# Kernel tuning notes

Hardware: AMD Instinct MI355X
Metric: run time of the kernel (lower is better)

Reference implementation:

```python
import jax, jax.numpy as jnp
import numpy as np
from jax import lax

# Model hyperparameters (match init_kwargs + Mamba2 defaults: ngroups=1, d_conv=4)
B_, IN_DIM, L_ = 4, 128, 2048
D_MODEL, OUT_DIM, D_STATE, K_SAME = 256, 128, 16, 4
EXPAND, HEADDIM, D_CONV = 3, 3, 4
D_INNER = EXPAND * D_MODEL            # 768
NHEADS = D_INNER // HEADDIM           # 256
CONV_DIM = D_INNER + 2 * D_STATE      # 800 (x, B, C go through depthwise conv)
D_IN_PROJ = 2 * D_INNER + 2 * D_STATE + NHEADS  # 1824 (z, xBC, dt)
EPS = 1e-5
DN = ('NCH', 'OIH', 'NCH')


def setup_inputs() -> dict:
    key = jax.random.key(0)
    ks = jax.random.split(key, 12)
    s = lambda f: 1.0 / np.sqrt(f)
    x = jax.random.normal(ks[0], (B_, IN_DIM, L_), jnp.float32)
    conv_w = jax.random.normal(ks[1], (D_MODEL, IN_DIM, K_SAME), jnp.float32) * s(IN_DIM * K_SAME)
    conv_b = jax.random.normal(ks[2], (D_MODEL,), jnp.float32) * 0.02
    in_proj_w = jax.random.normal(ks[3], (D_MODEL, D_IN_PROJ), jnp.float32) * s(D_MODEL)
    dw_conv_w = jax.random.normal(ks[4], (CONV_DIM, D_CONV), jnp.float32) * s(D_CONV)
    dw_conv_b = jax.random.normal(ks[5], (CONV_DIM,), jnp.float32) * 0.02
    dt_bias = jax.random.normal(ks[6], (NHEADS,), jnp.float32) * 0.5
    A_log = jnp.log(jax.random.uniform(ks[7], (NHEADS,), jnp.float32, 1.0, 16.0))
    D = 1.0 + jax.random.normal(ks[8], (NHEADS,), jnp.float32) * 0.1
    norm_w = jnp.ones((D_INNER,), jnp.float32)
    mamba_out_w = jax.random.normal(ks[9], (D_INNER, D_MODEL), jnp.float32) * s(D_INNER)
    out_conv_w = jax.random.normal(ks[10], (OUT_DIM, D_MODEL, K_SAME), jnp.float32) * s(D_MODEL * K_SAME)
    return dict(x=x, conv_w=conv_w, conv_b=conv_b, in_proj_w=in_proj_w,
                dw_conv_w=dw_conv_w, dw_conv_b=dw_conv_b, dt_bias=dt_bias,
                A_log=A_log, D=D, norm_w=norm_w, mamba_out_w=mamba_out_w,
                out_conv_w=out_conv_w)


def _ssd_scan(dt, A, Bm, Cm, xs):
    """Selective state-space recurrence.
    dt: [B,L,H]  A: [H]  Bm,Cm: [B,L,N]  xs: [B,L,H,P]  ->  y: [B,L,H,P]"""
    dA = jnp.exp(dt * A)  # [B,L,H]

    def step(h, inp):  # h: [B,H,P,N]
        dA_t, dt_t, B_t, C_t, x_t = inp
        dBx = (dt_t[:, :, None] * x_t)[..., None] * B_t[:, None, None, :]  # [B,H,P,N]
        h = h * dA_t[:, :, None, None] + dBx
        y = jnp.einsum('bhpn,bn->bhp', h, C_t)
        return h, y

    inputs = (dA.transpose(1, 0, 2), dt.transpose(1, 0, 2),
              Bm.transpose(1, 0, 2), Cm.transpose(1, 0, 2), xs.transpose(1, 0, 2, 3))
    h0 = jnp.zeros((dt.shape[0], NHEADS, HEADDIM, D_STATE), dt.dtype)
    _, ys = lax.scan(step, h0, inputs)
    return ys.transpose(1, 0, 2, 3)


def reference(x, conv_w, conv_b, in_proj_w, dw_conv_w, dw_conv_b, dt_bias,
              A_log, D, norm_w, mamba_out_w, out_conv_w):
    B, _, L = x.shape
    # Conv1d padding='same' with even kernel k=4: torch pads (left=1, right=2)
    h = lax.conv_general_dilated(x, conv_w, (1,), [(1, 2)], dimension_numbers=DN)
    h = h + conv_b[None, :, None]
    u = h.transpose(0, 2, 1)  # [B,L,d_model]

    zxbcdt = u @ in_proj_w  # [B,L,1824]
    z = zxbcdt[..., :D_INNER]
    xBC = zxbcdt[..., D_INNER:D_INNER + CONV_DIM]
    dt = zxbcdt[..., D_INNER + CONV_DIM:]  # [B,L,H]
    dt = jax.nn.softplus(dt + dt_bias)

    # causal depthwise conv over xBC, then silu
    xBC_c = lax.conv_general_dilated(xBC.transpose(0, 2, 1), dw_conv_w[:, None, :], (1,),
                                     [(D_CONV - 1, 0)], feature_group_count=CONV_DIM,
                                     dimension_numbers=DN)
    xBC = jax.nn.silu((xBC_c + dw_conv_b[None, :, None]).transpose(0, 2, 1))
    xs = xBC[..., :D_INNER].reshape(B, L, NHEADS, HEADDIM)
    Bm = xBC[..., D_INNER:D_INNER + D_STATE]
    Cm = xBC[..., D_INNER + D_STATE:]

    A = -jnp.exp(A_log)
    y = _ssd_scan(dt, A, Bm, Cm, xs) + D[None, None, :, None] * xs  # [B,L,H,P]
    y = y.reshape(B, L, D_INNER)

    # gated RMSNorm (norm_before_gate=False): gate first, then normalize
    y = y * jax.nn.silu(z)
    y = y * lax.rsqrt(jnp.mean(y * y, axis=-1, keepdims=True) + EPS) * norm_w

    out = (y @ mamba_out_w).transpose(0, 2, 1)  # [B,d_model,L]
    out = lax.conv_general_dilated(out, out_conv_w, (1,), [(1, 2)], dimension_numbers=DN)
    return out
```

## Files before the change

### kernel.cpp

```cpp
#include <hip/hip_runtime.h>
#include <math.h>

#define B_      4
#define L_      2048
#define IN_DIM  128
#define D_MODEL 256
#define OUT_DIM 128
#define D_STATE 16
#define D_INNER 768
#define NHEADS  256
#define HEADDIM 3
#define CONV_DIM 800
#define D_IN_PROJ 1824
#define DT_START (D_INNER + CONV_DIM)

#define SCAN_NC 32
#define SCAN_CL 64
#define LPAD    2051

typedef short  short8 __attribute__((ext_vector_type(8)));
typedef float  f32x4  __attribute__((ext_vector_type(4)));

__device__ __forceinline__ unsigned short f2bf(float f) {
    unsigned int u = __float_as_uint(f);
    u = (u + 0x7fffu + ((u >> 16) & 1u)) >> 16;
    return (unsigned short)u;
}
__device__ __forceinline__ float bf2f(unsigned short h) {
    return __uint_as_float(((unsigned int)h) << 16);
}

__global__ __launch_bounds__(256) void prep_early_kernel(
    unsigned short* __restrict__ xh, unsigned short* __restrict__ xl,
    const float* __restrict__ cw, unsigned short* __restrict__ cwh,
    unsigned short* __restrict__ cwl)
{
    if (blockIdx.x < 6) {
        int t = blockIdx.x * 256 + threadIdx.x;
        int n = B_ * 3 * IN_DIM;
        if (t < n) {
            int ch = t % IN_DIM, rb = t / IN_DIM;
            int b = rb / 3, ri = rb % 3;
            int row = (ri == 0) ? 0 : (ri == 1) ? (L_ + 1) : (L_ + 2);
            size_t off = ((size_t)b * LPAD + row) * IN_DIM + ch;
            xh[off] = 0; xl[off] = 0;
        }
    } else {
        int t = (blockIdx.x - 6) * 256 + threadIdx.x;
        if (t < D_MODEL * 512) {
            int o = t >> 9, kk = t & 511;
            int k = kk >> 7, i = kk & 127;
            float v = cw[((size_t)o * IN_DIM + i) * 4 + k];
            unsigned short h = f2bf(v);
            cwh[t] = h; cwl[t] = f2bf(v - bf2f(h));
        }
    }
}

__global__ __launch_bounds__(256) void prep_late_kernel(
    const float* __restrict__ cow, unsigned short* __restrict__ cowh,
    unsigned short* __restrict__ th)
{
    if (blockIdx.x < 512) {
        int t = blockIdx.x * 256 + threadIdx.x;
        if (t < OUT_DIM * 1024) {
            int o = t >> 10, kk = t & 1023;
            int k = kk >> 8, c = kk & 255;
            cowh[t] = f2bf(cow[((size_t)o * D_MODEL + c) * 4 + k]);
        }
    } else {
        int t = (blockIdx.x - 512) * 256 + threadIdx.x;
        int n = B_ * 3 * D_MODEL;
        if (t < n) {
            int ch = t % D_MODEL, rb = t / D_MODEL;
            int b = rb / 3, ri = rb % 3;
            int row = (ri == 0) ? 0 : (ri == 1) ? (L_ + 1) : (L_ + 2);
            size_t off = ((size_t)b * LPAD + row) * D_MODEL + ch;
            th[off] = 0;
        }
    }
}

__global__ __launch_bounds__(256) void transpose_x_kernel(
    const float* __restrict__ x, unsigned short* __restrict__ xh,
    unsigned short* __restrict__ xl)
{
    __shared__ float tile[32][33];
    int b = blockIdx.z;
    int l0 = blockIdx.x * 32, i0 = blockIdx.y * 32;
    int tx = threadIdx.x & 31, ty = threadIdx.x >> 5;
    const float* xb = x + (size_t)b * IN_DIM * L_;
    #pragma unroll
    for (int r = 0; r < 4; ++r)
        tile[ty + r * 8][tx] = xb[(size_t)(i0 + ty + r * 8) * L_ + l0 + tx];
    __syncthreads();
    #pragma unroll
    for (int r = 0; r < 4; ++r) {
        int l = l0 + ty + r * 8;
        float v = tile[tx][ty + r * 8];
        size_t off = ((size_t)b * LPAD + l + 1) * IN_DIM + i0 + tx;
        unsigned short h = f2bf(v);
        xh[off] = h;
        xl[off] = f2bf(v - bf2f(h));
    }
}

__global__ __launch_bounds__(256) void tconv_kernel(
    const float* __restrict__ src, unsigned short* __restrict__ dh,
    unsigned short* __restrict__ dl, int K, int N)
{
    __shared__ float tile[32][33];
    int k0 = blockIdx.y * 32, n0 = blockIdx.x * 32;
    int tx = threadIdx.x & 31, ty = threadIdx.x >> 5;
    #pragma unroll
    for (int r = 0; r < 4; ++r)
        tile[ty + r * 8][tx] = src[(size_t)(k0 + ty + r * 8) * N + n0 + tx];
    __syncthreads();
    #pragma unroll
    for (int r = 0; r < 4; ++r) {
        int n = n0 + ty + r * 8;
        float v = tile[tx][ty + r * 8];
        unsigned short h = f2bf(v);
        dh[(size_t)n * K + k0 + tx] = h;
        dl[(size_t)n * K + k0 + tx] = f2bf(v - bf2f(h));
    }
}

__global__ __launch_bounds__(256) void gemm_ip2_kernel(
    const unsigned short* __restrict__ Ah, const unsigned short* __restrict__ Al,
    const unsigned short* __restrict__ Bh, const unsigned short* __restrict__ Bl,
    float* __restrict__ C, int M, int N, int K)
{
    __shared__ __align__(16) unsigned short AsH[128][40];
    __shared__ __align__(16) unsigned short AsL[128][40];
    __shared__ __align__(16) unsigned short BsH[128][40];
    __shared__ __align__(16) unsigned short BsL[128][40];

    int m0 = blockIdx.y * 128, n0 = blockIdx.x * 128;
    int t = threadIdx.x;
    int wid = t >> 6, lane = t & 63;
    int wm = (wid >> 1) * 64, wn = (wid & 1) * 64;
    int fr = lane & 15, fq = lane >> 4;
    bool full = (n0 + 127 >= DT_START);

    f32x4 z4 = {0.f, 0.f, 0.f, 0.f};
    f32x4 acc[4][4];
    #pragma unroll
    for (int i = 0; i < 4; ++i)
        #pragma unroll
        for (int j = 0; j < 4; ++j) acc[i][j] = z4;

    if (!full) {
        for (int k0 = 0; k0 < K; k0 += 32) {
            __syncthreads();
            #pragma unroll
            for (int p = 0; p < 2; ++p) {
                int idx = p * 256 + t;
                int row = idx >> 2, q = idx & 3;
                int koff = k0 + q * 8;
                *(float4*)&AsH[row][q * 8] =
                    *(const float4*)(Ah + (size_t)(m0 + row) * K + koff);
                int n = n0 + row;
                *(float4*)&BsH[row][q * 8] =
                    *(const float4*)(Bh + (size_t)n * K + koff);
            }
            __syncthreads();

            short8 ah[4], bh[4];
            #pragma unroll
            for (int i = 0; i < 4; ++i) {
                ah[i] = *(const short8*)&AsH[wm + i * 16 + fr][fq * 8];
                bh[i] = *(const short8*)&BsH[wn + i * 16 + fr][fq * 8];
            }
            #pragma unroll
            for (int i = 0; i < 4; ++i)
                #pragma unroll
                for (int j = 0; j < 4; ++j)
                    acc[i][j] = __builtin_amdgcn_mfma_f32_16x16x32_bf16(
                        ah[i], bh[j], acc[i][j], 0, 0, 0);
        }
    } else {
        for (int k0 = 0; k0 < K; k0 += 32) {
            __syncthreads();
            #pragma unroll
            for (int p = 0; p < 2; ++p) {
                int idx = p * 256 + t;
                int row = idx >> 2, q = idx & 3;
                int koff = k0 + q * 8;
                *(float4*)&AsH[row][q * 8] =
                    *(const float4*)(Ah + (size_t)(m0 + row) * K + koff);
                *(float4*)&AsL[row][q * 8] =
                    *(const float4*)(Al + (size_t)(m0 + row) * K + koff);
                int n = n0 + row;
                float4 vbh = make_float4(0.f, 0.f, 0.f, 0.f), vbl = vbh;
                if (n < N) {
                    vbh = *(const float4*)(Bh + (size_t)n * K + koff);
                    vbl = *(const float4*)(Bl + (size_t)n * K + koff);
                }
                *(float4*)&BsH[row][q * 8] = vbh;
                *(float4*)&BsL[row][q * 8] = vbl;
            }
            __syncthreads();

            short8 ah[4], al[4], bh[4], bl[4];
            #pragma unroll
            for (int i = 0; i < 4; ++i) {
                ah[i] = *(const short8*)&AsH[wm + i * 16 + fr][fq * 8];
                al[i] = *(const short8*)&AsL[wm + i * 16 + fr][fq * 8];
                bh[i] = *(const short8*)&BsH[wn + i * 16 + fr][fq * 8];
                bl[i] = *(const short8*)&BsL[wn + i * 16 + fr][fq * 8];
            }
            #pragma unroll
            for (int i = 0; i < 4; ++i)
                #pragma unroll
                for (int j = 0; j < 4; ++j) {
                    acc[i][j] = __builtin_amdgcn_mfma_f32_16x16x32_bf16(
                        ah[i], bh[j], acc[i][j], 0, 0, 0);
                    acc[i][j] = __builtin_amdgcn_mfma_f32_16x16x32_bf16(
                        ah[i], bl[j], acc[i][j], 0, 0, 0);
                    acc[i][j] = __builtin_amdgcn_mfma_f32_16x16x32_bf16(
                        al[i], bh[j], acc[i][j], 0, 0, 0);
                }
        }
    }

    #pragma unroll
    for (int i = 0; i < 4; ++i) {
        int r0 = m0 + wm + i * 16 + fq * 4;
        #pragma unroll
        for (int j = 0; j < 4; ++j) {
            int cc = n0 + wn + j * 16 + fr;
            if (cc < N) {
                #pragma unroll
                for (int r = 0; r < 4; ++r)
                    C[(size_t)(r0 + r) * N + cc] = acc[i][j][r];
            }
        }
    }
}

__global__ __launch_bounds__(256) void gemm_ci_kernel(
    const unsigned short* __restrict__ Ah, const unsigned short* __restrict__ Al,
    const unsigned short* __restrict__ Bh, const unsigned short* __restrict__ Bl,
    const float* __restrict__ bias,
    unsigned short* __restrict__ Ch, unsigned short* __restrict__ Cl)
{
    const int K = 512;
    __shared__ __align__(16) unsigned short AsH[128][40];
    __shared__ __align__(16) unsigned short AsL[128][40];
    __shared__ __align__(16) unsigned short BsH[128][40];
    __shared__ __align__(16) unsigned short BsL[128][40];

    int m0 = blockIdx.y * 128, n0 = blockIdx.x * 128;
    int b = m0 >> 11;
    size_t abase = ((size_t)b * LPAD + (m0 & 2047)) * IN_DIM;
    int t = threadIdx.x;
    int wid = t >> 6, lane = t & 63;
    int wm = (wid >> 1) * 64, wn = (wid & 1) * 64;
    int fr = lane & 15, fq = lane >> 4;

    f32x4 z4 = {0.f, 0.f, 0.f, 0.f};
    f32x4 acc[4][4];
    #pragma unroll
    for (int i = 0; i < 4; ++i)
        #pragma unroll
        for (int j = 0; j < 4; ++j) acc[i][j] = z4;

    for (int k0 = 0; k0 < K; k0 += 32) {
        __syncthreads();
        #pragma unroll
        for (int p = 0; p < 2; ++p) {
            int idx = p * 256 + t;
            int row = idx >> 2, q = idx & 3;
            int koff = k0 + q * 8;
            *(float4*)&AsH[row][q * 8] =
                *(const float4*)(Ah + abase + (size_t)row * IN_DIM + koff);
            *(float4*)&AsL[row][q * 8] =
                *(const float4*)(Al + abase + (size_t)row * IN_DIM + koff);
            int n = n0 + row;
            *(float4*)&BsH[row][q * 8] = *(const float4*)(Bh + (size_t)n * K + koff);
            *(float4*)&BsL[row][q * 8] = *(const float4*)(Bl + (size_t)n * K + koff);
        }
        __syncthreads();

        short8 ah[4], al[4], bh[4], bl[4];
        #pragma unroll
        for (int i = 0; i < 4; ++i) {
            ah[i] = *(const short8*)&AsH[wm + i * 16 + fr][fq * 8];
            al[i] = *(const short8*)&AsL[wm + i * 16 + fr][fq * 8];
            bh[i] = *(const short8*)&BsH[wn + i * 16 + fr][fq * 8];
            bl[i] = *(const short8*)&BsL[wn + i * 16 + fr][fq * 8];
        }
        #pragma unroll
        for (int i = 0; i < 4; ++i)
            #pragma unroll
            for (int j = 0; j < 4; ++j) {
                acc[i][j] = __builtin_amdgcn_mfma_f32_16x16x32_bf16(
                    ah[i], bh[j], acc[i][j], 0, 0, 0);
                acc[i][j] = __builtin_amdgcn_mfma_f32_16x16x32_bf16(
                    ah[i], bl[j], acc[i][j], 0, 0, 0);
                acc[i][j] = __builtin_amdgcn_mfma_f32_16x16x32_bf16(
                    al[i], bh[j], acc[i][j], 0, 0, 0);
            }
    }

    #pragma unroll
    for (int i = 0; i < 4; ++i) {
        int r0 = m0 + wm + i * 16 + fq * 4;
        #pragma unroll
        for (int j = 0; j < 4; ++j) {
            int cc = n0 + wn + j * 16 + fr;
            float bc = bias[cc];
            #pragma unroll
            for (int r = 0; r < 4; ++r) {
                float v = acc[i][j][r] + bc;
                unsigned short h = f2bf(v);
                size_t off = (size_t)(r0 + r) * D_MODEL + cc;
                Ch[off] = h;
                Cl[off] = f2bf(v - bf2f(h));
            }
        }
    }
}

__global__ __launch_bounds__(256) void gemm_mo_kernel(
    const unsigned short* __restrict__ Ah, const unsigned short* __restrict__ Bh,
    unsigned short* __restrict__ Ch)
{
    const int K = D_INNER;
    __shared__ __align__(16) unsigned short AsH[128][40];
    __shared__ __align__(16) unsigned short BsH[128][40];

    int m0 = blockIdx.y * 128, n0 = blockIdx.x * 128;
    int t = threadIdx.x;
    int wid = t >> 6, lane = t & 63;
    int wm = (wid >> 1) * 64, wn = (wid & 1) * 64;
    int fr = lane & 15, fq = lane >> 4;

    f32x4 z4 = {0.f, 0.f, 0.f, 0.f};
    f32x4 acc[4][4];
    #pragma unroll
    for (int i = 0; i < 4; ++i)
        #pragma unroll
        for (int j = 0; j < 4; ++j) acc[i][j] = z4;

    for (int k0 = 0; k0 < K; k0 += 32) {
        __syncthreads();
        #pragma unroll
        for (int p = 0; p < 2; ++p) {
            int idx = p * 256 + t;
            int row = idx >> 2, q = idx & 3;
            int koff = k0 + q * 8;
            *(float4*)&AsH[row][q * 8] =
                *(const float4*)(Ah + (size_t)(m0 + row) * K + koff);
            int n = n0 + row;
            *(float4*)&BsH[row][q * 8] = *(const float4*)(Bh + (size_t)n * K + koff);
        }
        __syncthreads();

        short8 ah[4], bh[4];
        #pragma unroll
        for (int i = 0; i < 4; ++i) {
            ah[i] = *(const short8*)&AsH[wm + i * 16 + fr][fq * 8];
            bh[i] = *(const short8*)&BsH[wn + i * 16 + fr][fq * 8];
        }
        #pragma unroll
        for (int i = 0; i < 4; ++i)
            #pragma unroll
            for (int j = 0; j < 4; ++j)
                acc[i][j] = __builtin_amdgcn_mfma_f32_16x16x32_bf16(
                    ah[i], bh[j], acc[i][j], 0, 0, 0);
    }

    int b = m0 >> 11;
    #pragma unroll
    for (int i = 0; i < 4; ++i) {
        int r0 = m0 + wm + i * 16 + fq * 4;
        #pragma unroll
        for (int j = 0; j < 4; ++j) {
            int cc = n0 + wn + j * 16 + fr;
            #pragma unroll
            for (int r = 0; r < 4; ++r) {
                int l = (r0 + r) & 2047;
                size_t off = ((size_t)b * LPAD + l + 1) * D_MODEL + cc;
                Ch[off] = f2bf(acc[i][j][r]);
            }
        }
    }
}

__global__ __launch_bounds__(256) void gemm_co_kernel(
    const unsigned short* __restrict__ Ah, const unsigned short* __restrict__ Bh,
    float* __restrict__ out)
{
    const int K = 1024;
    __shared__ __align__(16) unsigned short AsH[128][40];
    __shared__ __align__(16) unsigned short BsH[128][40];

    int m0 = blockIdx.y * 128;
    int b = m0 >> 11, l0t = m0 & 2047;
    size_t abase = ((size_t)b * LPAD + l0t) * D_MODEL;
    int t = threadIdx.x;
    int wid = t >> 6, lane = t & 63;
    int wm = (wid >> 1) * 64, wn = (wid & 1) * 64;
    int fr = lane & 15, fq = lane >> 4;

    f32x4 z4 = {0.f, 0.f, 0.f, 0.f};
    f32x4 acc[4][4];
    #pragma unroll
    for (int i = 0; i < 4; ++i)
        #pragma unroll
        for (int j = 0; j < 4; ++j) acc[i][j] = z4;

    for (int k0 = 0; k0 < K; k0 += 32) {
        __syncthreads();
        #pragma unroll
        for (int p = 0; p < 2; ++p) {
            int idx = p * 256 + t;
            int row = idx >> 2, q = idx & 3;
            int koff = k0 + q * 8;
            *(float4*)&AsH[row][q * 8] =
                *(const float4*)(Ah + abase + (size_t)row * D_MODEL + koff);
            *(float4*)&BsH[row][q * 8] = *(const float4*)(Bh + (size_t)row * K + koff);
        }
        __syncthreads();

        short8 ah[4], bh[4];
        #pragma unroll
        for (int i = 0; i < 4; ++i) {
            ah[i] = *(const short8*)&AsH[wm + i * 16 + fr][fq * 8];
            bh[i] = *(const short8*)&BsH[wn + i * 16 + fr][fq * 8];
        }
        #pragma unroll
        for (int i = 0; i < 4; ++i)
            #pragma unroll
            for (int j = 0; j < 4; ++j)
                acc[i][j] = __builtin_amdgcn_mfma_f32_16x16x32_bf16(
                    ah[i], bh[j], acc[i][j], 0, 0, 0);
    }

    #pragma unroll
    for (int i = 0; i < 4; ++i) {
        int lr = l0t + wm + i * 16 + fq * 4;
        #pragma unroll
        for (int j = 0; j < 4; ++j) {
            int cc = wn + j * 16 + fr;
            float* dst = out + ((size_t)(b * OUT_DIM + cc)) * L_ + lr;
            float4 ov = make_float4(acc[i][j][0], acc[i][j][1],
                                    acc[i][j][2], acc[i][j][3]);
            *(float4*)dst = ov;
        }
    }
}

__global__ __launch_bounds__(256) void dwconv_kernel(
    const float* __restrict__ zx, const float* __restrict__ w,
    const float* __restrict__ bias, float* __restrict__ xBCs)
{
    int idx = blockIdx.x * 256 + threadIdx.x;
    int c   = idx % CONV_DIM;
    int bl8 = idx / CONV_DIM;
    int b  = bl8 >> 8;
    int l0 = (bl8 & 255) * 8;
    float4 wv = *(const float4*)&w[c * 4];
    float bi = bias[c];
    const float* base = zx + ((size_t)(b * L_ + l0)) * D_IN_PROJ + D_INNER + c;
    float r[11];
    #pragma unroll
    for (int k = 0; k < 11; ++k) {
        int l = l0 - 3 + k;
        r[k] = (l >= 0) ? base[(ptrdiff_t)(k - 3) * D_IN_PROJ] : 0.f;
    }
    #pragma unroll
    for (int i = 0; i < 8; ++i) {
        float acc = bi;
        acc = fmaf(r[i + 0], wv.x, acc);
        acc = fmaf(r[i + 1], wv.y, acc);
        acc = fmaf(r[i + 2], wv.z, acc);
        acc = fmaf(r[i + 3], wv.w, acc);
        float s = acc / (1.f + expf(-acc));
        xBCs[((size_t)(b * L_ + l0 + i)) * CONV_DIM + c] = s;
    }
}

__global__ __launch_bounds__(256) void gmat_kernel(
    const float* __restrict__ xBCs, float* __restrict__ G)
{
    __shared__ float Bs[64][16];
    __shared__ float Cs[64][16];
    int c = blockIdx.x & 31, b = blockIdx.x >> 5;
    int t = threadIdx.x;
    int row0 = b * L_ + c * SCAN_CL;
    {
        int j = t >> 2, q = t & 3;
        const float* r = xBCs + (size_t)(row0 + j) * CONV_DIM + D_INNER;
        *(float4*)&Bs[j][q * 4] = *(const float4*)(r + q * 4);
        *(float4*)&Cs[j][q * 4] = *(const float4*)(r + D_STATE + q * 4);
    }
    __syncthreads();
    int i = t >> 2, jq = t & 3;
    float4 c0 = *(const float4*)&Cs[i][0];
    float4 c1 = *(const float4*)&Cs[i][4];
    float4 c2 = *(const float4*)&Cs[i][8];
    float4 c3 = *(const float4*)&Cs[i][12];
    float dot[16];
    #pragma unroll
    for (int jj = 0; jj < 16; ++jj) {
        int j = jq * 16 + jj;
        float4 b0 = *(const float4*)&Bs[j][0];
        float4 b1 = *(const float4*)&Bs[j][4];
        float4 b2 = *(const float4*)&Bs[j][8];
        float4 b3 = *(const float4*)&Bs[j][12];
        float d = c0.x * b0.x + c0.y * b0.y + c0.z * b0.z + c0.w * b0.w;
        d = fmaf(c1.x, b1.x, d); d = fmaf(c1.y, b1.y, d);
        d = fmaf(c1.z, b1.z, d); d = fmaf(c1.w, b1.w, d);
        d = fmaf(c2.x, b2.x, d); d = fmaf(c2.y, b2.y, d);
        d = fmaf(c2.z, b2.z, d); d = fmaf(c2.w, b2.w, d);
        d = fmaf(c3.x, b3.x, d); d = fmaf(c3.y, b3.y, d);
        d = fmaf(c3.z, b3.z, d); d = fmaf(c3.w, b3.w, d);
        dot[jj] = d;
    }
    float* gout = G + ((size_t)blockIdx.x * 64 + i) * 64 + jq * 16;
    #pragma unroll
    for (int q = 0; q < 4; ++q)
        *(float4*)(gout + q * 4) = make_float4(dot[q*4], dot[q*4+1], dot[q*4+2], dot[q*4+3]);
}

__device__ __forceinline__ void scan_decode(int bid, int& b, int& c, int& hg)
{
    int bcl = bid & 7;
    hg = (bid >> 3) & 31;
    int bc = ((bid >> 8) << 3) | bcl;
    c = bc & 31;
    b = bc >> 5;
}

__global__ __launch_bounds__(512) void scan_local2(
    const float* __restrict__ xBCs, const float* __restrict__ zx,
    const float* __restrict__ dt_bias, const float* __restrict__ A_log,
    float* __restrict__ Sloc, float* __restrict__ prodA,
    float* __restrict__ dtb)
{
    __shared__ float  BsT[16][68];
    __shared__ __align__(16) float4 PkC4L[8][66];
    __shared__ float  UT[8][3][64];
    int b, c, hg;
    scan_decode(blockIdx.x, b, c, hg);
    int h0 = hg * 8;
    int t = threadIdx.x;
    int row0 = b * L_ + c * SCAN_CL;

    if (t < 256) {
        int j = t >> 2, q = t & 3;
        const float* r = xBCs + (size_t)(row0 + j) * CONV_DIM;
        float4 bv = *(const float4*)(r + D_INNER + q * 4);
        BsT[q*4+0][j] = bv.x; BsT[q*4+1][j] = bv.y;
        BsT[q*4+2][j] = bv.z; BsT[q*4+3][j] = bv.w;
    }
    {
        int hh = t & 7, j = t >> 3;
        float v = zx[(size_t)(row0 + j) * D_IN_PROJ + DT_START + h0 + hh]
                  + dt_bias[h0 + hh];
        float dtv = (v > 20.f) ? v : log1pf(expf(v));
        dtb[(size_t)(row0 + j) * NHEADS + h0 + hh] = dtv;
        const float* xr = xBCs + (size_t)(row0 + j) * CONV_DIM + (h0 + hh) * 3;
        PkC4L[hh][j] = make_float4(dtv * xr[0], dtv * xr[1], dtv * xr[2], dtv);
    }
    __syncthreads();

    int wv = t >> 6, lane = t & 63;
    int hh = wv;
    int hhu = __builtin_amdgcn_readfirstlane(wv);
    int p = lane >> 4, n = lane & 15;
    int pc = (p < 3) ? p : 2;

    float4 own = PkC4L[hh][lane];
    float pkx = own.x, pky = own.y, pkz = own.z, pkw = own.w;
    float A = -__expf(A_log[h0 + hhu]);
    float cum = pkw * A;
    #pragma unroll
    for (int off = 1; off < 64; off <<= 1) {
        float sv = __shfl_up(cum, off);
        if (lane >= off) cum += sv;
    }
    float cum63 = __shfl(cum, 63);
    float wf = __expf(cum63 - cum);
    UT[hh][0][lane] = wf * pkx;
    UT[hh][1][lane] = wf * pky;
    UT[hh][2][lane] = wf * pkz;
    float state = 0.f;
    #pragma unroll
    for (int q = 0; q < 16; ++q) {
        float4 Bv = *(const float4*)&BsT[n][q * 4];
        float4 Uv = *(const float4*)&UT[hh][pc][q * 4];
        state = fmaf(Uv.x, Bv.x, state);
        state = fmaf(Uv.y, Bv.y, state);
        state = fmaf(Uv.z, Bv.z, state);
        state = fmaf(Uv.w, Bv.w, state);
    }
    size_t bh = (size_t)(b * NHEADS + h0 + hh);
    if (p < 3) Sloc[(bh * SCAN_NC + c) * 48 + p * 16 + n] = state;
    if (lane == 0) prodA[bh * SCAN_NC + c] = __expf(cum63);
}

__global__ __launch_bounds__(256) void scan_prefix_kernel(
    float* __restrict__ Sloc, const float* __restrict__ prodA)
{
    int wv   = blockIdx.x * 4 + (threadIdx.x >> 6);
    int lane = threadIdx.x & 63;
    int p = lane >> 4, n = lane & 15;
    bool act = (p < 3);
    int l48 = ((p < 3) ? p : 2) * 16 + n;
    size_t base = (size_t)wv * SCAN_NC;

    float cur = 0.f;
    for (int c = 0; c < SCAN_NC; ++c) {
        float s  = Sloc[(base + c) * 48 + l48];
        float pa = prodA[base + c];
        if (act) Sloc[(base + c) * 48 + l48] = cur;
        cur = fmaf(pa, cur, s);
    }
}

__global__ __launch_bounds__(512) void scan_final2(
    const float* __restrict__ xBCs, const float* __restrict__ dtb,
    const float* __restrict__ A_log, const float* __restrict__ Dp,
    const float* __restrict__ Sinit, const float* __restrict__ G,
    float* __restrict__ y)
{
    __shared__ __align__(16) float4 PkC4[8][68];
    __shared__ float XWx[8][68];
    __shared__ float XWy[8][68];
    __shared__ float XWz[8][68];
    __shared__ __align__(16) float Cs[64][34];
    union GsYsr {
        float gs[64][66];
        float ysr[64][25];
    };
    __shared__ __align__(16) GsYsr Us;
    int b, c, hg;
    scan_decode(blockIdx.x, b, c, hg);
    int h0 = hg * 8;
    int t = threadIdx.x;
    int row0 = b * L_ + c * SCAN_CL;

    {
        int hh = t & 7, j = t >> 3;
        float dtv = dtb[(size_t)(row0 + j) * NHEADS + h0 + hh];
        const float* xr = xBCs + (size_t)(row0 + j) * CONV_DIM + (h0 + hh) * 3;
        PkC4[hh][j + (j >> 4)] =
            make_float4(dtv * xr[0], dtv * xr[1], dtv * xr[2], dtv);
    }
    if (t < 256) {
        int j = t >> 2, q = t & 3;
        const float* r = xBCs + (size_t)(row0 + j) * CONV_DIM + D_INNER + D_STATE;
        *(float4*)&Cs[j][q * 4] = *(const float4*)(r + q * 4);
    }
    {
        const float* Gsrc = G + (size_t)(b * SCAN_NC + c) * 4096;
        #pragma unroll
        for (int e = 0; e < 2; ++e) {
            int idx = e * 512 + t;
            int row = idx >> 4, cq = (idx & 15) * 4;
            *(float4*)&Us.gs[row][cq] = *(const float4*)(Gsrc + (size_t)idx * 4);
        }
    }
    __syncthreads();

    int wv = t >> 6, lane = t & 63;
    int hh = wv;
    int hhu = __builtin_amdgcn_readfirstlane(wv);
    int I = lane >> 4;

    float4 own = PkC4[hh][lane + (lane >> 4)];
    float pkx = own.x, pky = own.y, pkz = own.z, pkw = own.w;

    const float* sinp = Sinit +
        ((size_t)(b * NHEADS + h0 + hhu) * SCAN_NC + c) * 48;
    float A = -__expf(A_log[h0 + hhu]);
    float Dh = Dp[h0 + hhu];

    float cum = pkw * A;
    #pragma unroll
    for (int off = 1; off < 64; off <<= 1) {
        float sv = __shfl_up(cum, off);
        if (lane >= off) cum += sv;
    }
    float e0 = __shfl(cum, 15);
    float e1 = __shfl(cum, 31);
    float e2 = __shfl(cum, 47);
    float e3 = __shfl(cum, 63);
    int ia = (I << 4) - 1;
    float AIr = __shfl(cum, ia < 0 ? 0 : ia);
    float AI = (I == 0) ? 0.f : AIr;
    float ri = __expf(cum - AI);
    float Eo = (I == 0) ? e0 : (I == 1) ? e1 : (I == 2) ? e2 : e3;
    float wj = __expf(Eo - cum);
    XWx[hh][lane] = wj * pkx;
    XWy[hh][lane] = wj * pky;
    XWz[hh][lane] = wj * pkz;
    PkC4[hh][lane + (lane >> 4)].w = cum;
    float S0 = (I > 0) ? __expf(AI - e0) : 0.f;
    float S1 = (I > 1) ? __expf(AI - e1) : 0.f;
    float S2 = (I > 2) ? __expf(AI - e2) : 0.f;
    float ecum = __expf(cum);

    float4 c0 = *(const float4*)&Cs[lane][0];
    float4 c1 = *(const float4*)&Cs[lane][4];
    float4 c2 = *(const float4*)&Cs[lane][8];
    float4 c3 = *(const float4*)&Cs[lane][12];

    float s0, s1, s2;
    {
        s0 = c0.x*sinp[0];  s0 = fmaf(c0.y,sinp[1],s0);  s0 = fmaf(c0.z,sinp[2],s0);  s0 = fmaf(c0.w,sinp[3],s0);
        s0 = fmaf(c1.x,sinp[4],s0);  s0 = fmaf(c1.y,sinp[5],s0);  s0 = fmaf(c1.z,sinp[6],s0);  s0 = fmaf(c1.w,sinp[7],s0);
        s0 = fmaf(c2.x,sinp[8],s0);  s0 = fmaf(c2.y,sinp[9],s0);  s0 = fmaf(c2.z,sinp[10],s0); s0 = fmaf(c2.w,sinp[11],s0);
        s0 = fmaf(c3.x,sinp[12],s0); s0 = fmaf(c3.y,sinp[13],s0); s0 = fmaf(c3.z,sinp[14],s0); s0 = fmaf(c3.w,sinp[15],s0);
        s1 = c0.x*sinp[16]; s1 = fmaf(c0.y,sinp[17],s1); s1 = fmaf(c0.z,sinp[18],s1); s1 = fmaf(c0.w,sinp[19],s1);
        s1 = fmaf(c1.x,sinp[20],s1); s1 = fmaf(c1.y,sinp[21],s1); s1 = fmaf(c1.z,sinp[22],s1); s1 = fmaf(c1.w,sinp[23],s1);
        s1 = fmaf(c2.x,sinp[24],s1); s1 = fmaf(c2.y,sinp[25],s1); s1 = fmaf(c2.z,sinp[26],s1); s1 = fmaf(c2.w,sinp[27],s1);
        s1 = fmaf(c3.x,sinp[28],s1); s1 = fmaf(c3.y,sinp[29],s1); s1 = fmaf(c3.z,sinp[30],s1); s1 = fmaf(c3.w,sinp[31],s1);
        s2 = c0.x*sinp[32]; s2 = fmaf(c0.y,sinp[33],s2); s2 = fmaf(c0.z,sinp[34],s2); s2 = fmaf(c0.w,sinp[35],s2);
        s2 = fmaf(c1.x,sinp[36],s2); s2 = fmaf(c1.y,sinp[37],s2); s2 = fmaf(c1.z,sinp[38],s2); s2 = fmaf(c1.w,sinp[39],s2);
        s2 = fmaf(c2.x,sinp[40],s2); s2 = fmaf(c2.y,sinp[41],s2); s2 = fmaf(c2.z,sinp[42],s2); s2 = fmaf(c2.w,sinp[43],s2);
        s2 = fmaf(c3.x,sinp[44],s2); s2 = fmaf(c3.y,sinp[45],s2); s2 = fmaf(c3.z,sinp[46],s2); s2 = fmaf(c3.w,sinp[47],s2);
    }

    float acc0 = 0.f, acc1 = 0.f, acc2 = 0.f;
    #pragma unroll
    for (int J = 0; J < 3; ++J) {
        float SJ = (J == 0) ? S0 : (J == 1) ? S1 : S2;
        float t0 = 0.f, t1 = 0.f, t2 = 0.f;
        #pragma unroll
        for (int q = 0; q < 4; ++q) {
            float4 g4 = *(const float4*)&Us.gs[lane][J * 16 + q * 4];
            float4 ux = *(const float4*)&XWx[hh][J * 16 + q * 4];
            float4 uy = *(const float4*)&XWy[hh][J * 16 + q * 4];
            float4 uz = *(const float4*)&XWz[hh][J * 16 + q * 4];
            t0 = fmaf(g4.x, ux.x, t0); t1 = fmaf(g4.x, uy.x, t1); t2 = fmaf(g4.x, uz.x, t2);
            t0 = fmaf(g4.y, ux.y, t0); t1 = fmaf(g4.y, uy.y, t1); t2 = fmaf(g4.y, uz.y, t2);
            t0 = fmaf(g4.z, ux.z, t0); t1 = fmaf(g4.z, uy.z, t1); t2 = fmaf(g4.z, uz.z, t2);
            t0 = fmaf(g4.w, ux.w, t0); t1 = fmaf(g4.w, uy.w, t1); t2 = fmaf(g4.w, uz.w, t2);
        }
        acc0 = fmaf(SJ, t0, acc0);
        acc1 = fmaf(SJ, t1, acc1);
        acc2 = fmaf(SJ, t2, acc2);
    }

    float d0 = 0.f, d1 = 0.f, d2 = 0.f;
    const float4* pkr = &PkC4[hh][I * 17];
    int lr = lane & 15;
    #pragma unroll
    for (int q = 0; q < 4; ++q) {
        float4 g4 = *(const float4*)&Us.gs[lane][(I << 4) + q * 4];
        #pragma unroll
        for (int k = 0; k < 4; ++k) {
            int kk = q * 4 + k;
            float4 p4 = pkr[kk];
            float gk = (k == 0) ? g4.x : (k == 1) ? g4.y : (k == 2) ? g4.z : g4.w;
            float e = __expf(cum - p4.w);
            float mg = (kk <= lr) ? e * gk : 0.f;
            d0 = fmaf(mg, p4.x, d0);
            d1 = fmaf(mg, p4.y, d1);
            d2 = fmaf(mg, p4.z, d2);
        }
    }

    float rdt = 1.0f / pkw;
    float y0 = fmaf(ri, acc0, d0) + fmaf(ecum, s0, Dh * (pkx * rdt));
    float y1 = fmaf(ri, acc1, d1) + fmaf(ecum, s1, Dh * (pky * rdt));
    float y2 = fmaf(ri, acc2, d2) + fmaf(ecum, s2, Dh * (pkz * rdt));

    __syncthreads();
    {
        float* yr = &Us.ysr[lane][hh * 3];
        yr[0] = y0; yr[1] = y1; yr[2] = y2;
    }
    __syncthreads();

    {
        int i2 = t >> 3, q2 = t & 7;
        float* dst = y + (size_t)(row0 + i2) * D_INNER + hg * 24 + q2 * 3;
        dst[0] = Us.ysr[i2][q2 * 3 + 0];
        dst[1] = Us.ysr[i2][q2 * 3 + 1];
        dst[2] = Us.ysr[i2][q2 * 3 + 2];
    }
}

__global__ __launch_bounds__(256) void gate_norm_kernel(
    const float* __restrict__ zx, const float* __restrict__ norm_w,
    const float* __restrict__ y, unsigned short* __restrict__ yh)
{
    int bl = blockIdx.x;
    int t  = threadIdx.x;
    const float* zrow = zx + (size_t)bl * D_IN_PROJ;
    const float* yrow = y + (size_t)bl * D_INNER;

    float v[3];
    float ss = 0.f;
    #pragma unroll
    for (int j = 0; j < 3; ++j) {
        int i = t + j * 256;
        float z = zrow[i];
        float s = z / (1.f + expf(-z));
        float val = yrow[i] * s;
        v[j] = val;
        ss += val * val;
    }
    ss += __shfl_xor(ss, 32);
    ss += __shfl_xor(ss, 16);
    ss += __shfl_xor(ss, 8);
    ss += __shfl_xor(ss, 4);
    ss += __shfl_xor(ss, 2);
    ss += __shfl_xor(ss, 1);
    __shared__ float red[4];
    int lane = t & 63, wid = t >> 6;
    if (lane == 0) red[wid] = ss;
    __syncthreads();
    float tot = red[0] + red[1] + red[2] + red[3];
    float rs = rsqrtf(tot * (1.f / D_INNER) + 1e-5f);
    #pragma unroll
    for (int j = 0; j < 3; ++j) {
        int i = t + j * 256;
        float o = v[j] * rs * norm_w[i];
        yh[(size_t)bl * D_INNER + i] = f2bf(o);
    }
}

extern "C" void kernel_launch(void* const* d_in, const int* in_sizes, int n_in,
                              void* d_out, int out_size, void* d_ws, size_t ws_size,
                              hipStream_t stream)
{
    const float* x           = (const float*)d_in[0];
    const float* conv_w      = (const float*)d_in[1];
    const float* conv_b      = (const float*)d_in[2];
    const float* in_proj_w   = (const float*)d_in[3];
    const float* dw_conv_w   = (const float*)d_in[4];
    const float* dw_conv_b   = (const float*)d_in[5];
    const float* dt_bias     = (const float*)d_in[6];
    const float* A_log       = (const float*)d_in[7];
    const float* Dp          = (const float*)d_in[8];
    const float* norm_w      = (const float*)d_in[9];
    const float* mamba_out_w = (const float*)d_in[10];
    const float* out_conv_w  = (const float*)d_in[11];
    float* out = (float*)d_out;
    float* ws  = (float*)d_ws;

    float* S0   = ws;
    float* zx   = S0 + 2097152;
    float* xBCs = zx + 14942208;
    float* dtb  = xBCs + 6553600;
    float* ybuf = dtb + 2097152;

    float* Gbuf = S0;
    float* Sloc = S0 + 524288;
    unsigned short* cow_hi = (unsigned short*)S0;

    unsigned short* xT_hi = (unsigned short*)zx;
    unsigned short* xT_lo = (unsigned short*)(zx + 525056);
    unsigned short* cw_hi = (unsigned short*)(zx + 1050112);
    unsigned short* cw_lo = (unsigned short*)(zx + 1115648);
    unsigned short* tmpP_hi = (unsigned short*)zx;
    unsigned short* mow_hi  = (unsigned short*)(zx + 2100224);
    unsigned short* mow_lo  = (unsigned short*)(zx + 2198528);

    unsigned short* ipw_hi = (unsigned short*)xBCs;
    unsigned short* ipw_lo = (unsigned short*)(xBCs + 233472);
    unsigned short* yb_hi  = (unsigned short*)xBCs;

    float* prodA = ybuf;
    unsigned short* u_hi = (unsigned short*)(ybuf + 32768);
    unsigned short* u_lo = (unsigned short*)(ybuf + 32768 + 1048576);

    prep_early_kernel<<<518, 256, 0, stream>>>(xT_hi, xT_lo, conv_w, cw_hi, cw_lo);
    transpose_x_kernel<<<dim3(L_ / 32, IN_DIM / 32, B_), 256, 0, stream>>>(
        x, xT_hi, xT_lo);
    gemm_ci_kernel<<<dim3(2, (B_ * L_) / 128), 256, 0, stream>>>(
        xT_hi, xT_lo, cw_hi, cw_lo, conv_b, u_hi, u_lo);

    tconv_kernel<<<dim3(D_IN_PROJ / 32, D_MODEL / 32), 256, 0, stream>>>(
        in_proj_w, ipw_hi, ipw_lo, D_MODEL, D_IN_PROJ);
    gemm_ip2_kernel<<<dim3((D_IN_PROJ + 127) / 128, (B_ * L_) / 128), 256, 0, stream>>>(
        u_hi, u_lo, ipw_hi, ipw_lo, zx, B_ * L_, D_IN_PROJ, D_MODEL);

    dwconv_kernel<<<(B_ * (L_ / 8) * CONV_DIM) / 256, 256, 0, stream>>>(
        zx, dw_conv_w, dw_conv_b, xBCs);
    gmat_kernel<<<B_ * SCAN_NC, 256, 0, stream>>>(xBCs, Gbuf);
    scan_local2<<<B_ * SCAN_NC * (NHEADS / 8), 512, 0, stream>>>(
        xBCs, zx, dt_bias, A_log, Sloc, prodA, dtb);
    scan_prefix_kernel<<<(B_ * NHEADS) / 4, 256, 0, stream>>>(Sloc, prodA);
    scan_final2<<<B_ * SCAN_NC * (NHEADS / 8), 512, 0, stream>>>(
        xBCs, dtb, A_log, Dp, Sloc, Gbuf, ybuf);

    gate_norm_kernel<<<B_ * L_, 256, 0, stream>>>(zx, norm_w, ybuf, yb_hi);

    prep_late_kernel<<<524, 256, 0, stream>>>(out_conv_w, cow_hi, tmpP_hi);
    tconv_kernel<<<dim3(D_MODEL / 32, D_INNER / 32), 256, 0, stream>>>(
        mamba_out_w, mow_hi, mow_lo, D_INNER, D_MODEL);
    gemm_mo_kernel<<<dim3(2, (B_ * L_) / 128), 256, 0, stream>>>(
        yb_hi, mow_hi, tmpP_hi);

    gemm_co_kernel<<<dim3(1, (B_ * L_) / 128), 256, 0, stream>>>(
        tmpP_hi, cow_hi, out);
}
```

Baseline: 274.7 us.

## Merge prep, transpose and gmat launches into fewer kernels; swizzle scan LDS

Three prep and transpose kernels (input-conv weight split, x transpose, in_proj weight transpose) become one launch dispatched by block index, and the output-side prep plus the mamba_out weight transpose become another. The gmat B·C Gram kernel is folded into scan_local2 as 128 extra leading blocks. Together these cut launch count and the idle gaps between dependent kernels. Separately, scan_final2 drops the padding on the G tile in shared memory and uses an XOR swizzle on the column index, which changes the bank-conflict pattern of the float4 reads. In exchange, the gmat blocks now run at 512-thread granularity with half the threads idle, and shared-memory use per block grows in the fused scan kernel.

```diff
diff --git a/kernel.cpp b/kernel.cpp
--- a/kernel.cpp
+++ b/kernel.cpp
@@ -30,13 +30,18 @@
     return __uint_as_float(((unsigned int)h) << 16);
 }
 
-__global__ __launch_bounds__(256) void prep_early_kernel(
+__global__ __launch_bounds__(256) void prep_all_kernel(
     unsigned short* __restrict__ xh, unsigned short* __restrict__ xl,
     const float* __restrict__ cw, unsigned short* __restrict__ cwh,
-    unsigned short* __restrict__ cwl)
-{
-    if (blockIdx.x < 6) {
-        int t = blockIdx.x * 256 + threadIdx.x;
+    unsigned short* __restrict__ cwl,
+    const float* __restrict__ x,
+    const float* __restrict__ ipsrc, unsigned short* __restrict__ ipwh,
+    unsigned short* __restrict__ ipwl)
+{
+    __shared__ float tile[32][33];
+    int bid = blockIdx.x;
+    if (bid < 6) {
+        int t = bid * 256 + threadIdx.x;
         int n = B_ * 3 * IN_DIM;
         if (t < n) {
             int ch = t % IN_DIM, rb = t / IN_DIM;
@@ -45,8 +50,8 @@
             size_t off = ((size_t)b * LPAD + row) * IN_DIM + ch;
             xh[off] = 0; xl[off] = 0;
         }
-    } else {
-        int t = (blockIdx.x - 6) * 256 + threadIdx.x;
+    } else if (bid < 518) {
+        int t = (bid - 6) * 256 + threadIdx.x;
         if (t < D_MODEL * 512) {
             int o = t >> 9, kk = t & 511;
             int k = kk >> 7, i = kk & 127;
@@ -54,22 +59,62 @@
             unsigned short h = f2bf(v);
             cwh[t] = h; cwl[t] = f2bf(v - bf2f(h));
         }
-    }
-}
-
-__global__ __launch_bounds__(256) void prep_late_kernel(
+    } else if (bid < 1542) {
+        int tid = bid - 518;
+        int b = tid >> 8;
+        int l0 = (tid & 63) * 32, i0 = ((tid >> 6) & 3) * 32;
+        int tx = threadIdx.x & 31, ty = threadIdx.x >> 5;
+        const float* xb = x + (size_t)b * IN_DIM * L_;
+        #pragma unroll
+        for (int r = 0; r < 4; ++r)
+            tile[ty + r * 8][tx] = xb[(size_t)(i0 + ty + r * 8) * L_ + l0 + tx];
+        __syncthreads();
+        #pragma unroll
+        for (int r = 0; r < 4; ++r) {
+            int l = l0 + ty + r * 8;
+            float v = tile[tx][ty + r * 8];
+            size_t off = ((size_t)b * LPAD + l + 1) * IN_DIM + i0 + tx;
+            unsigned short h = f2bf(v);
+            xh[off] = h;
+            xl[off] = f2bf(v - bf2f(h));
+        }
+    } else {
+        int tid = bid - 1542;
+        int n0 = (tid % 57) * 32, k0 = (tid / 57) * 32;
+        const int K = D_MODEL, N = D_IN_PROJ;
+        int tx = threadIdx.x & 31, ty = threadIdx.x >> 5;
+        #pragma unroll
+        for (int r = 0; r < 4; ++r)
+            tile[ty + r * 8][tx] = ipsrc[(size_t)(k0 + ty + r * 8) * N + n0 + tx];
+        __syncthreads();
+        #pragma unroll
+        for (int r = 0; r < 4; ++r) {
+            int n = n0 + ty + r * 8;
+            float v = tile[tx][ty + r * 8];
+            unsigned short h = f2bf(v);
+            ipwh[(size_t)n * K + k0 + tx] = h;
+            ipwl[(size_t)n * K + k0 + tx] = f2bf(v - bf2f(h));
+        }
+    }
+}
+
+__global__ __launch_bounds__(256) void prep_late2_kernel(
     const float* __restrict__ cow, unsigned short* __restrict__ cowh,
-    unsigned short* __restrict__ th)
-{
-    if (blockIdx.x < 512) {
-        int t = blockIdx.x * 256 + threadIdx.x;
+    unsigned short* __restrict__ th,
+    const float* __restrict__ mosrc, unsigned short* __restrict__ mowh,
+    unsigned short* __restrict__ mowl)
+{
+    __shared__ float tile[32][33];
+    int bid = blockIdx.x;
+    if (bid < 512) {
+        int t = bid * 256 + threadIdx.x;
         if (t < OUT_DIM * 1024) {
             int o = t >> 10, kk = t & 1023;
             int k = kk >> 8, c = kk & 255;
             cowh[t] = f2bf(cow[((size_t)o * D_MODEL + c) * 4 + k]);
         }
-    } else {
-        int t = (blockIdx.x - 512) * 256 + threadIdx.x;
+    } else if (bid < 524) {
+        int t = (bid - 512) * 256 + threadIdx.x;
         int n = B_ * 3 * D_MODEL;
         if (t < n) {
             int ch = t % D_MODEL, rb = t / D_MODEL;
@@ -78,51 +123,23 @@
             size_t off = ((size_t)b * LPAD + row) * D_MODEL + ch;
             th[off] = 0;
         }
-    }
-}
-
-__global__ __launch_bounds__(256) void transpose_x_kernel(
-    const float* __restrict__ x, unsigned short* __restrict__ xh,
-    unsigned short* __restrict__ xl)
-{
-    __shared__ float tile[32][33];
-    int b = blockIdx.z;
-    int l0 = blockIdx.x * 32, i0 = blockIdx.y * 32;
-    int tx = threadIdx.x & 31, ty = threadIdx.x >> 5;
-    const float* xb = x + (size_t)b * IN_DIM * L_;
-    #pragma unroll
-    for (int r = 0; r < 4; ++r)
-        tile[ty + r * 8][tx] = xb[(size_t)(i0 + ty + r * 8) * L_ + l0 + tx];
-    __syncthreads();
-    #pragma unroll
-    for (int r = 0; r < 4; ++r) {
-        int l = l0 + ty + r * 8;
-        float v = tile[tx][ty + r * 8];
-        size_t off = ((size_t)b * LPAD + l + 1) * IN_DIM + i0 + tx;
-        unsigned short h = f2bf(v);
-        xh[off] = h;
-        xl[off] = f2bf(v - bf2f(h));
-    }
-}
-
-__global__ __launch_bounds__(256) void tconv_kernel(
-    const float* __restrict__ src, unsigned short* __restrict__ dh,
-    unsigned short* __restrict__ dl, int K, int N)
-{
-    __shared__ float tile[32][33];
-    int k0 = blockIdx.y * 32, n0 = blockIdx.x * 32;
-    int tx = threadIdx.x & 31, ty = threadIdx.x >> 5;
-    #pragma unroll
-    for (int r = 0; r < 4; ++r)
-        tile[ty + r * 8][tx] = src[(size_t)(k0 + ty + r * 8) * N + n0 + tx];
-    __syncthreads();
-    #pragma unroll
-    for (int r = 0; r < 4; ++r) {
-        int n = n0 + ty + r * 8;
-        float v = tile[tx][ty + r * 8];
-        unsigned short h = f2bf(v);
-        dh[(size_t)n * K + k0 + tx] = h;
-        dl[(size_t)n * K + k0 + tx] = f2bf(v - bf2f(h));
+    } else {
+        int tid = bid - 524;
+        int n0 = (tid & 7) * 32, k0 = (tid >> 3) * 32;
+        const int K = D_INNER, N = D_MODEL;
+        int tx = threadIdx.x & 31, ty = threadIdx.x >> 5;
+        #pragma unroll
+        for (int r = 0; r < 4; ++r)
+            tile[ty + r * 8][tx] = mosrc[(size_t)(k0 + ty + r * 8) * N + n0 + tx];
+        __syncthreads();
+        #pragma unroll
+        for (int r = 0; r < 4; ++r) {
+            int n = n0 + ty + r * 8;
+            float v = tile[tx][ty + r * 8];
+            unsigned short h = f2bf(v);
+            mowh[(size_t)n * K + k0 + tx] = h;
+            mowl[(size_t)n * K + k0 + tx] = f2bf(v - bf2f(h));
+        }
     }
 }
 
@@ -483,49 +500,6 @@
     }
 }
 
-__global__ __launch_bounds__(256) void gmat_kernel(
-    const float* __restrict__ xBCs, float* __restrict__ G)
-{
-    __shared__ float Bs[64][16];
-    __shared__ float Cs[64][16];
-    int c = blockIdx.x & 31, b = blockIdx.x >> 5;
-    int t = threadIdx.x;
-    int row0 = b * L_ + c * SCAN_CL;
-    {
-        int j = t >> 2, q = t & 3;
-        const float* r = xBCs + (size_t)(row0 + j) * CONV_DIM + D_INNER;
-        *(float4*)&Bs[j][q * 4] = *(const float4*)(r + q * 4);
-        *(float4*)&Cs[j][q * 4] = *(const float4*)(r + D_STATE + q * 4);
-    }
-    __syncthreads();
-    int i = t >> 2, jq = t & 3;
-    float4 c0 = *(const float4*)&Cs[i][0];
-    float4 c1 = *(const float4*)&Cs[i][4];
-    float4 c2 = *(const float4*)&Cs[i][8];
-    float4 c3 = *(const float4*)&Cs[i][12];
-    float dot[16];
-    #pragma unroll
-    for (int jj = 0; jj < 16; ++jj) {
-        int j = jq * 16 + jj;
-        float4 b0 = *(const float4*)&Bs[j][0];
-        float4 b1 = *(const float4*)&Bs[j][4];
-        float4 b2 = *(const float4*)&Bs[j][8];
-        float4 b3 = *(const float4*)&Bs[j][12];
-        float d = c0.x * b0.x + c0.y * b0.y + c0.z * b0.z + c0.w * b0.w;
-        d = fmaf(c1.x, b1.x, d); d = fmaf(c1.y, b1.y, d);
-        d = fmaf(c1.z, b1.z, d); d = fmaf(c1.w, b1.w, d);
-        d = fmaf(c2.x, b2.x, d); d = fmaf(c2.y, b2.y, d);
-        d = fmaf(c2.z, b2.z, d); d = fmaf(c2.w, b2.w, d);
-        d = fmaf(c3.x, b3.x, d); d = fmaf(c3.y, b3.y, d);
-        d = fmaf(c3.z, b3.z, d); d = fmaf(c3.w, b3.w, d);
-        dot[jj] = d;
-    }
-    float* gout = G + ((size_t)blockIdx.x * 64 + i) * 64 + jq * 16;
-    #pragma unroll
-    for (int q = 0; q < 4; ++q)
-        *(float4*)(gout + q * 4) = make_float4(dot[q*4], dot[q*4+1], dot[q*4+2], dot[q*4+3]);
-}
-
 __device__ __forceinline__ void scan_decode(int bid, int& b, int& c, int& hg)
 {
     int bcl = bid & 7;
@@ -535,19 +509,64 @@
     b = bc >> 5;
 }
 
-__global__ __launch_bounds__(512) void scan_local2(
+__global__ __launch_bounds__(512) void scan_local2g(
     const float* __restrict__ xBCs, const float* __restrict__ zx,
     const float* __restrict__ dt_bias, const float* __restrict__ A_log,
     float* __restrict__ Sloc, float* __restrict__ prodA,
-    float* __restrict__ dtb)
-{
+    float* __restrict__ dtb, float* __restrict__ G)
+{
+    int bid = blockIdx.x;
+    int t = threadIdx.x;
+    if (bid < 128) {
+        __shared__ float Bs[64][16];
+        __shared__ float Csg[64][16];
+        int c = bid & 31, b = bid >> 5;
+        int row0 = b * L_ + c * SCAN_CL;
+        if (t < 256) {
+            int j = t >> 2, q = t & 3;
+            const float* r = xBCs + (size_t)(row0 + j) * CONV_DIM + D_INNER;
+            *(float4*)&Bs[j][q * 4] = *(const float4*)(r + q * 4);
+            *(float4*)&Csg[j][q * 4] = *(const float4*)(r + D_STATE + q * 4);
+        }
+        __syncthreads();
+        if (t < 256) {
+            int i = t >> 2, jq = t & 3;
+            float4 c0 = *(const float4*)&Csg[i][0];
+            float4 c1 = *(const float4*)&Csg[i][4];
+            float4 c2 = *(const float4*)&Csg[i][8];
+            float4 c3 = *(const float4*)&Csg[i][12];
+            float dot[16];
+            #pragma unroll
+            for (int jj = 0; jj < 16; ++jj) {
+                int j = jq * 16 + jj;
+                float4 b0 = *(const float4*)&Bs[j][0];
+                float4 b1 = *(const float4*)&Bs[j][4];
+                float4 b2 = *(const float4*)&Bs[j][8];
+                float4 b3 = *(const float4*)&Bs[j][12];
+                float d = c0.x * b0.x + c0.y * b0.y + c0.z * b0.z + c0.w * b0.w;
+                d = fmaf(c1.x, b1.x, d); d = fmaf(c1.y, b1.y, d);
+                d = fmaf(c1.z, b1.z, d); d = fmaf(c1.w, b1.w, d);
+                d = fmaf(c2.x, b2.x, d); d = fmaf(c2.y, b2.y, d);
+                d = fmaf(c2.z, b2.z, d); d = fmaf(c2.w, b2.w, d);
+                d = fmaf(c3.x, b3.x, d); d = fmaf(c3.y, b3.y, d);
+                d = fmaf(c3.z, b3.z, d); d = fmaf(c3.w, b3.w, d);
+                dot[jj] = d;
+            }
+            float* gout = G + ((size_t)bid * 64 + i) * 64 + jq * 16;
+            #pragma unroll
+            for (int q = 0; q < 4; ++q)
+                *(float4*)(gout + q * 4) =
+                    make_float4(dot[q*4], dot[q*4+1], dot[q*4+2], dot[q*4+3]);
+        }
+        return;
+    }
+
     __shared__ float  BsT[16][68];
     __shared__ __align__(16) float4 PkC4L[8][66];
     __shared__ float  UT[8][3][64];
     int b, c, hg;
-    scan_decode(blockIdx.x, b, c, hg);
+    scan_decode(bid - 128, b, c, hg);
     int h0 = hg * 8;
-    int t = threadIdx.x;
     int row0 = b * L_ + c * SCAN_CL;
 
     if (t < 256) {
@@ -628,13 +647,13 @@
     const float* __restrict__ Sinit, const float* __restrict__ G,
     float* __restrict__ y)
 {
-    __shared__ __align__(16) float4 PkC4[8][68];
-    __shared__ float XWx[8][68];
-    __shared__ float XWy[8][68];
-    __shared__ float XWz[8][68];
-    __shared__ __align__(16) float Cs[64][34];
+    __shared__ __align__(16) float4 PkC4[8][67];
+    __shared__ float XWx[8][64];
+    __shared__ float XWy[8][64];
+    __shared__ float XWz[8][64];
+    __shared__ __align__(16) float Cs[64][36];
     union GsYsr {
-        float gs[64][66];
+        float gs[64][64];
         float ysr[64][25];
     };
     __shared__ __align__(16) GsYsr Us;
@@ -662,7 +681,8 @@
         for (int e = 0; e < 2; ++e) {
             int idx = e * 512 + t;
             int row = idx >> 4, cq = (idx & 15) * 4;
-            *(float4*)&Us.gs[row][cq] = *(const float4*)(Gsrc + (size_t)idx * 4);
+            *(float4*)&Us.gs[row][cq ^ ((row & 7) << 2)] =
+                *(const float4*)(Gsrc + (size_t)idx * 4);
         }
     }
     __syncthreads();
@@ -671,6 +691,7 @@
     int hh = wv;
     int hhu = __builtin_amdgcn_readfirstlane(wv);
     int I = lane >> 4;
+    int sw = (lane & 7) << 2;
 
     float4 own = PkC4[hh][lane + (lane >> 4)];
     float pkx = own.x, pky = own.y, pkz = own.z, pkw = own.w;
@@ -733,7 +754,7 @@
         float t0 = 0.f, t1 = 0.f, t2 = 0.f;
         #pragma unroll
         for (int q = 0; q < 4; ++q) {
-            float4 g4 = *(const float4*)&Us.gs[lane][J * 16 + q * 4];
+            float4 g4 = *(const float4*)&Us.gs[lane][(J * 16 + q * 4) ^ sw];
             float4 ux = *(const float4*)&XWx[hh][J * 16 + q * 4];
             float4 uy = *(const float4*)&XWy[hh][J * 16 + q * 4];
             float4 uz = *(const float4*)&XWz[hh][J * 16 + q * 4];
@@ -752,7 +773,7 @@
     int lr = lane & 15;
     #pragma unroll
     for (int q = 0; q < 4; ++q) {
-        float4 g4 = *(const float4*)&Us.gs[lane][(I << 4) + q * 4];
+        float4 g4 = *(const float4*)&Us.gs[lane][((I << 4) + q * 4) ^ sw];
         #pragma unroll
         for (int k = 0; k < 4; ++k) {
             int kk = q * 4 + k;
@@ -872,31 +893,28 @@
     unsigned short* u_hi = (unsigned short*)(ybuf + 32768);
     unsigned short* u_lo = (unsigned short*)(ybuf + 32768 + 1048576);
 
-    prep_early_kernel<<<518, 256, 0, stream>>>(xT_hi, xT_lo, conv_w, cw_hi, cw_lo);
-    transpose_x_kernel<<<dim3(L_ / 32, IN_DIM / 32, B_), 256, 0, stream>>>(
-        x, xT_hi, xT_lo);
+    prep_all_kernel<<<1998, 256, 0, stream>>>(
+        xT_hi, xT_lo, conv_w, cw_hi, cw_lo, x, in_proj_w, ipw_hi, ipw_lo);
+
     gemm_ci_kernel<<<dim3(2, (B_ * L_) / 128), 256, 0, stream>>>(
         xT_hi, xT_lo, cw_hi, cw_lo, conv_b, u_hi, u_lo);
 
-    tconv_kernel<<<dim3(D_IN_PROJ / 32, D_MODEL / 32), 256, 0, stream>>>(
-        in_proj_w, ipw_hi, ipw_lo, D_MODEL, D_IN_PROJ);
     gemm_ip2_kernel<<<dim3((D_IN_PROJ + 127) / 128, (B_ * L_) / 128), 256, 0, stream>>>(
         u_hi, u_lo, ipw_hi, ipw_lo, zx, B_ * L_, D_IN_PROJ, D_MODEL);
 
     dwconv_kernel<<<(B_ * (L_ / 8) * CONV_DIM) / 256, 256, 0, stream>>>(
         zx, dw_conv_w, dw_conv_b, xBCs);
-    gmat_kernel<<<B_ * SCAN_NC, 256, 0, stream>>>(xBCs, Gbuf);
-    scan_local2<<<B_ * SCAN_NC * (NHEADS / 8), 512, 0, stream>>>(
-        xBCs, zx, dt_bias, A_log, Sloc, prodA, dtb);
+    scan_local2g<<<128 + B_ * SCAN_NC * (NHEADS / 8), 512, 0, stream>>>(
+        xBCs, zx, dt_bias, A_log, Sloc, prodA, dtb, Gbuf);
     scan_prefix_kernel<<<(B_ * NHEADS) / 4, 256, 0, stream>>>(Sloc, prodA);
     scan_final2<<<B_ * SCAN_NC * (NHEADS / 8), 512, 0, stream>>>(
         xBCs, dtb, A_log, Dp, Sloc, Gbuf, ybuf);
 
     gate_norm_kernel<<<B_ * L_, 256, 0, stream>>>(zx, norm_w, ybuf, yb_hi);
 
-    prep_late_kernel<<<524, 256, 0, stream>>>(out_conv_w, cow_hi, tmpP_hi);
-    tconv_kernel<<<dim3(D_MODEL / 32, D_INNER / 32), 256, 0, stream>>>(
-        mamba_out_w, mow_hi, mow_lo, D_INNER, D_MODEL);
+    prep_late2_kernel<<<716, 256, 0, stream>>>(
+        out_conv_w, cow_hi, tmpP_hi, mamba_out_w, mow_hi, mow_lo);
+
     gemm_mo_kernel<<<dim3(2, (B_ * L_) / 128), 256, 0, stream>>>(
         yb_hi, mow_hi, tmpP_hi);
 
```

After: 269.5 us. About the same (-1.9%).
